# Kernel tuning notes

Measured on AMD Instinct MI355X. Metric: run time of the kernel, lower is better.

Reference implementation:

```python
import jax, jax.numpy as jnp
import numpy as np
import math

D_MODEL = 1024
N_HEAD = 16
D_K = D_MODEL // N_HEAD  # 64
SEQ = 1024
BATCH = 8


def setup_inputs() -> dict:
    k = jax.random.key(0)
    ks = jax.random.split(k, 11)
    f32 = jnp.float32
    scale = 1.0 / math.sqrt(D_MODEL)
    return {
        "query": jax.random.normal(ks[0], (BATCH, SEQ, D_MODEL), dtype=f32),
        "key": jax.random.normal(ks[1], (BATCH, SEQ, D_MODEL), dtype=f32),
        "value": jax.random.normal(ks[2], (BATCH, SEQ, D_MODEL), dtype=f32),
        # Shaw-style relative position table a[q_pos, k_pos, d_k]
        "rel": jax.random.normal(ks[3], (SEQ, SEQ, D_K), dtype=f32) * 0.02,
        "W_q": jax.random.normal(ks[4], (D_MODEL, D_MODEL), dtype=f32) * scale,
        "b_q": jnp.zeros((D_MODEL,), dtype=f32),
        "W_k": jax.random.normal(ks[5], (D_MODEL, D_MODEL), dtype=f32) * scale,
        "b_k": jnp.zeros((D_MODEL,), dtype=f32),
        "W_v": jax.random.normal(ks[6], (D_MODEL, D_MODEL), dtype=f32) * scale,
        "b_v": jnp.zeros((D_MODEL,), dtype=f32),
        # boolean mask: True = masked out (matches torch masked_fill semantics)
        "mask": jax.random.randint(ks[7], (BATCH, SEQ, SEQ), 0, 4) == 0,
    }


def reference(query, key, value, rel, W_q, b_q, W_k, b_k, W_v, b_v, mask):
    B, S, D = query.shape
    H, dk = N_HEAD, D // N_HEAD

    def proj(x, W, b):
        # [B,S,D] -> [B,H,S,dk]
        return (x @ W + b).reshape(B, S, H, dk).transpose(0, 2, 1, 3)

    Q = proj(query, W_q, b_q)
    K = proj(key, W_k, b_k)
    V = proj(value, W_v, b_v)

    # E_1 = Q K^T / sqrt(d_k): [B,H,Sq,Sk]
    scores = jnp.einsum("bhqd,bhkd->bhqk", Q, K) / math.sqrt(dk)
    # E_2 = Q x relative_position (per query position), added UNscaled as in source
    scores = scores + jnp.einsum("bhqd,qkd->bhqk", Q, rel)
    # masked_fill(mask, -1e8)
    scores = jnp.where(mask[:, None, :, :], jnp.float32(-1e8), scores)
    attn = jax.nn.softmax(scores, axis=-1)
    out = jnp.einsum("bhqk,bhkd->bhqd", attn, V)  # [B,H,S,dk]
    return out.transpose(0, 2, 1, 3).reshape(B, S, D)
```

## Files before the change

kernel.cpp:

```cpp
#include <hip/hip_runtime.h>

typedef _Float16 h8_t __attribute__((ext_vector_type(8)));
typedef _Float16 h4_t __attribute__((ext_vector_type(4)));
typedef float f4_t __attribute__((ext_vector_type(4)));

#define MFMA16(a, b, c) __builtin_amdgcn_mfma_f32_16x16x32_f16((a), (b), (c), 0, 0, 0)

__global__ void cvt4(const float* __restrict__ in, _Float16* __restrict__ out, int n4) {
    int i = blockIdx.x * 256 + threadIdx.x;
    if (i < n4) {
        f4_t v = *(const f4_t*)(in + (size_t)i * 4);
        h4_t h;
        for (int j = 0; j < 4; ++j) h[j] = (_Float16)v[j];
        *(h4_t*)(out + (size_t)i * 4) = h;
    }
}

__global__ void wtrans(const float* __restrict__ W, _Float16* __restrict__ Wt) {
    __shared__ float tile[32][33];
    int tid = threadIdx.x;
    int tx = tid & 31, ty = tid >> 5;
    int nb = blockIdx.x * 32, kb = blockIdx.y * 32;
    for (int p = 0; p < 4; ++p)
        tile[ty + p * 8][tx] = W[(size_t)(kb + ty + p * 8) * 1024 + nb + tx];
    __syncthreads();
    for (int p = 0; p < 4; ++p)
        Wt[(size_t)(nb + ty + p * 8) * 1024 + kb + tx] = (_Float16)tile[tx][ty + p * 8];
}

__global__ __launch_bounds__(256, 2) void proj_gemm(
    const _Float16* __restrict__ X, const _Float16* __restrict__ Wt,
    const float* __restrict__ bias, _Float16* __restrict__ Out,
    float scale, int vmode)
{
    __shared__ __align__(16) _Float16 Asm[128][40];
    __shared__ __align__(16) _Float16 Bsm[128][40];
    int tid = threadIdx.x;
    int wave = tid >> 6, lane = tid & 63;
    int l15 = lane & 15, quad = lane >> 4;
    int m0 = blockIdx.x * 128, n0 = blockIdx.y * 128;
    int wm = (wave >> 1) * 64, wn = (wave & 1) * 64;
    f4_t acc[4][4] = {};
    int srow = tid >> 1, skoff = (tid & 1) * 16;

    for (int kt = 0; kt < 1024; kt += 32) {
        h8_t a0 = *(const h8_t*)&X[(size_t)(m0 + srow) * 1024 + kt + skoff];
        h8_t a1 = *(const h8_t*)&X[(size_t)(m0 + srow) * 1024 + kt + skoff + 8];
        h8_t b0 = *(const h8_t*)&Wt[(size_t)(n0 + srow) * 1024 + kt + skoff];
        h8_t b1 = *(const h8_t*)&Wt[(size_t)(n0 + srow) * 1024 + kt + skoff + 8];
        *(h8_t*)&Asm[srow][skoff] = a0;
        *(h8_t*)&Asm[srow][skoff + 8] = a1;
        *(h8_t*)&Bsm[srow][skoff] = b0;
        *(h8_t*)&Bsm[srow][skoff + 8] = b1;
        __syncthreads();
        h8_t af[4], bf[4];
        for (int i = 0; i < 4; ++i) af[i] = *(const h8_t*)&Asm[wm + i * 16 + l15][quad * 8];
        for (int j = 0; j < 4; ++j) bf[j] = *(const h8_t*)&Bsm[wn + j * 16 + l15][quad * 8];
        for (int i = 0; i < 4; ++i)
            for (int j = 0; j < 4; ++j)
                acc[i][j] = MFMA16(af[i], bf[j], acc[i][j]);
        __syncthreads();
    }
    for (int j = 0; j < 4; ++j) {
        int n = n0 + wn + j * 16 + l15;
        float bv = bias[n];
        int h = n >> 6, d = n & 63;
        for (int i = 0; i < 4; ++i) {
            for (int r = 0; r < 4; ++r) {
                int m = m0 + wm + i * 16 + quad * 4 + r;
                int bb = m >> 10, ss = m & 1023;
                float v = (acc[i][j][r] + bv) * scale;
                size_t oidx = vmode ? (((size_t)(bb * 16 + h) * 64 + d) * 1024 + ss)
                                    : (((size_t)(bb * 16 + h) * 1024 + ss) * 64 + d);
                Out[oidx] = (_Float16)v;
            }
        }
    }
}

__device__ inline h8_t ld_rel(const _Float16* relh, const float* relf, size_t idx) {
    if (relh) return *(const h8_t*)(relh + idx);
    f4_t a = *(const f4_t*)(relf + idx);
    f4_t b = *(const f4_t*)(relf + idx + 4);
    h8_t h;
    for (int j = 0; j < 4; ++j) { h[j] = (_Float16)a[j]; h[4 + j] = (_Float16)b[j]; }
    return h;
}

__global__ __launch_bounds__(256, 2) void attn_kernel(
    const _Float16* __restrict__ Qh,
    const _Float16* __restrict__ Kh,
    const _Float16* __restrict__ Vt,
    const _Float16* __restrict__ relh,
    const float* __restrict__ relf,
    const int* __restrict__ mask,
    float* __restrict__ out)
{
    __shared__ __align__(16) _Float16 R_lds[16][17][36];
    __shared__ __align__(16) _Float16 P_lds[16][16][40];

    const int tid = threadIdx.x;
    const int wave = tid >> 6, lane = tid & 63;
    const int l15 = lane & 15, quad = lane >> 4;
    const int b = blockIdx.y;
    const int q0 = blockIdx.x * 16;

    h8_t bQ[4][2];
    h8_t bR[4][2];
    for (int gi = 0; gi < 4; ++gi) {
        int g = wave * 4 + gi;
        const _Float16* qp = Qh + ((size_t)(b * 16 + g) * 1024 + q0 + l15) * 64 + quad * 8;
        bQ[gi][0] = *(const h8_t*)qp;
        bQ[gi][1] = *(const h8_t*)(qp + 32);
    }
    for (int qi = 0; qi < 4; ++qi) {
        int q = q0 + wave * 4 + qi;
        const _Float16* qp = Qh + ((size_t)(b * 16 + l15) * 1024 + q) * 64 + quad * 8;
        bR[qi][0] = *(const h8_t*)qp;
        bR[qi][1] = *(const h8_t*)(qp + 32);
    }

    f4_t acc[4][4] = {};
    float mst[4], lst[4];
    for (int gi = 0; gi < 4; ++gi) { mst[gi] = -1e30f; lst[gi] = 0.0f; }

    for (int t0 = 0; t0 < 1024; t0 += 32) {
        for (int qi = 0; qi < 4; ++qi) {
            int q = q0 + wave * 4 + qi;
            for (int tm = 0; tm < 2; ++tm) {
                f4_t c = {0.f, 0.f, 0.f, 0.f};
                size_t ridx = ((size_t)q * 1024 + t0 + tm * 16 + l15) * 64 + quad * 8;
                c = MFMA16(ld_rel(relh, relf, ridx), bR[qi][0], c);
                c = MFMA16(ld_rel(relh, relf, ridx + 32), bR[qi][1], c);
                h4_t h;
                for (int r = 0; r < 4; ++r) h[r] = (_Float16)c[r];
                *(h4_t*)&R_lds[wave * 4 + qi][l15][tm * 16 + quad * 4] = h;
            }
        }
        __syncthreads();

        int4 mk0 = *(const int4*)&mask[((size_t)b * 1024 + q0 + l15) * 1024 + t0 + quad * 4];
        int4 mk1 = *(const int4*)&mask[((size_t)b * 1024 + q0 + l15) * 1024 + t0 + 16 + quad * 4];
        int mm[8] = {mk0.x, mk0.y, mk0.z, mk0.w, mk1.x, mk1.y, mk1.z, mk1.w};

        for (int gi = 0; gi < 4; ++gi) {
            int g = wave * 4 + gi;
            f4_t s[2];
            for (int tm = 0; tm < 2; ++tm) {
                h4_t rh = *(const h4_t*)&R_lds[l15][g][tm * 16 + quad * 4];
                f4_t c;
                for (int r = 0; r < 4; ++r) c[r] = (float)rh[r];
                const _Float16* kp =
                    Kh + ((size_t)(b * 16 + g) * 1024 + t0 + tm * 16 + l15) * 64 + quad * 8;
                c = MFMA16(*(const h8_t*)kp, bQ[gi][0], c);
                c = MFMA16(*(const h8_t*)(kp + 32), bQ[gi][1], c);
                s[tm] = c;
            }
            for (int tm = 0; tm < 2; ++tm)
                for (int r = 0; r < 4; ++r)
                    if (mm[tm * 4 + r]) s[tm][r] = -1e8f;

            float mx = s[0][0];
            for (int tm = 0; tm < 2; ++tm)
                for (int r = 0; r < 4; ++r) mx = fmaxf(mx, s[tm][r]);
            mx = fmaxf(mx, __shfl_xor(mx, 16));
            mx = fmaxf(mx, __shfl_xor(mx, 32));
            float mnew = fmaxf(mst[gi], mx);
            float alpha = __expf(mst[gi] - mnew);
            mst[gi] = mnew;
            float rs = 0.0f;
            for (int tm = 0; tm < 2; ++tm)
                for (int r = 0; r < 4; ++r) {
                    float p = __expf(s[tm][r] - mnew);
                    s[tm][r] = p;
                    rs += p;
                }
            rs += __shfl_xor(rs, 16);
            rs += __shfl_xor(rs, 32);
            lst[gi] = lst[gi] * alpha + rs;
            for (int dm = 0; dm < 4; ++dm) acc[gi][dm] *= alpha;
            for (int tm = 0; tm < 2; ++tm) {
                h4_t h;
                for (int r = 0; r < 4; ++r) h[r] = (_Float16)s[tm][r];
                *(h4_t*)&P_lds[g][l15][tm * 16 + quad * 4] = h;
            }
        }
        __syncthreads();

        for (int gi = 0; gi < 4; ++gi) {
            int g = wave * 4 + gi;
            h8_t bp = *(const h8_t*)&P_lds[g][l15][quad * 8];
            const _Float16* vp = Vt + (size_t)(b * 16 + g) * 64 * 1024 + t0 + quad * 8;
            for (int dm = 0; dm < 4; ++dm) {
                h8_t av = *(const h8_t*)(vp + (size_t)(dm * 16 + l15) * 1024);
                acc[gi][dm] = MFMA16(av, bp, acc[gi][dm]);
            }
        }
    }

    for (int gi = 0; gi < 4; ++gi) {
        int g = wave * 4 + gi;
        float linv = 1.0f / lst[gi];
        for (int dm = 0; dm < 4; ++dm) {
            f4_t v = acc[gi][dm] * linv;
            float* op = out + ((size_t)b * 1024 + q0 + l15) * 1024 + g * 64 + dm * 16 + quad * 4;
            *(f4_t*)op = v;
        }
    }
}

extern "C" void kernel_launch(void* const* d_in, const int* in_sizes, int n_in,
                              void* d_out, int out_size, void* d_ws, size_t ws_size,
                              hipStream_t stream) {
    const float* q    = (const float*)d_in[0];
    const float* k    = (const float*)d_in[1];
    const float* v    = (const float*)d_in[2];
    const float* rel  = (const float*)d_in[3];
    const float* Wq   = (const float*)d_in[4];
    const float* bq   = (const float*)d_in[5];
    const float* Wk   = (const float*)d_in[6];
    const float* bk   = (const float*)d_in[7];
    const float* Wv   = (const float*)d_in[8];
    const float* bv   = (const float*)d_in[9];
    const int*   mask = (const int*)d_in[10];
    float* out = (float*)d_out;

    const size_t NEL = 8ull * 1024 * 1024;
    const size_t WEL = 1024ull * 1024;
    const size_t RELE = 1024ull * 1024 * 64;

    char* w = (char*)d_ws;
    size_t off = 0;
    auto alloc = [&](size_t bytes) { char* p = w + off; off += bytes; return p; };
    _Float16* qx  = (_Float16*)alloc(NEL * 2);
    _Float16* kx  = (_Float16*)alloc(NEL * 2);
    _Float16* vx  = (_Float16*)alloc(NEL * 2);
    _Float16* Wqt = (_Float16*)alloc(WEL * 2);
    _Float16* Wkt = (_Float16*)alloc(WEL * 2);
    _Float16* Wvt = (_Float16*)alloc(WEL * 2);
    _Float16* Qh  = (_Float16*)alloc(NEL * 2);
    _Float16* Kh  = (_Float16*)alloc(NEL * 2);
    _Float16* Vth = (_Float16*)alloc(NEL * 2);
    _Float16* relh = nullptr;
    if (ws_size >= off + RELE * 2) relh = (_Float16*)alloc(RELE * 2);

    cvt4<<<(int)(NEL / 4 / 256), 256, 0, stream>>>(q, qx, (int)(NEL / 4));
    cvt4<<<(int)(NEL / 4 / 256), 256, 0, stream>>>(k, kx, (int)(NEL / 4));
    cvt4<<<(int)(NEL / 4 / 256), 256, 0, stream>>>(v, vx, (int)(NEL / 4));
    if (relh)
        cvt4<<<(int)(RELE / 4 / 256), 256, 0, stream>>>(rel, relh, (int)(RELE / 4));

    dim3 tg(32, 32);
    wtrans<<<tg, 256, 0, stream>>>(Wq, Wqt);
    wtrans<<<tg, 256, 0, stream>>>(Wk, Wkt);
    wtrans<<<tg, 256, 0, stream>>>(Wv, Wvt);

    dim3 pg(64, 8);
    proj_gemm<<<pg, 256, 0, stream>>>(qx, Wqt, bq, Qh, 1.0f, 0);
    proj_gemm<<<pg, 256, 0, stream>>>(kx, Wkt, bk, Kh, 0.125f, 0);
    proj_gemm<<<pg, 256, 0, stream>>>(vx, Wvt, bv, Vth, 1.0f, 1);

    dim3 ag(64, 8);
    attn_kernel<<<ag, 256, 0, stream>>>(Qh, Kh, Vth, relh, rel, mask, out);
}
```

Baseline: 1.067 ms.

## Prefetch attention operands, double-buffer R tile, use direct global-to-LDS loads in projection

In the attention kernel, the mask, relative-position, K and V tiles are now loaded into registers in batches ahead of the MFMAs that use them. The R scratch buffer is double-buffered, which lets the barrier before the P·V step go, since each wave only reads back its own P rows. This is meant to expose more memory-level parallelism and cut barrier stalls on a loop that is bound by loads. The projection GEMM switches to global_load_lds with an unpadded 32-wide LDS layout. That removes the register round trip but may add LDS bank conflicts on the fragment reads, and the extra prefetch registers raise register pressure.

```diff
diff --git a/kernel.cpp b/kernel.cpp
--- a/kernel.cpp
+++ b/kernel.cpp
@@ -5,6 +5,12 @@
 typedef float f4_t __attribute__((ext_vector_type(4)));
 
 #define MFMA16(a, b, c) __builtin_amdgcn_mfma_f32_16x16x32_f16((a), (b), (c), 0, 0, 0)
+
+__device__ inline void gl_lds16(const _Float16* g, _Float16* l) {
+    __builtin_amdgcn_global_load_lds(
+        (const __attribute__((address_space(1))) unsigned int*)g,
+        (__attribute__((address_space(3))) unsigned int*)l, 16, 0, 0);
+}
 
 __global__ void cvt4(const float* __restrict__ in, _Float16* __restrict__ out, int n4) {
     int i = blockIdx.x * 256 + threadIdx.x;
@@ -33,29 +39,27 @@
     const float* __restrict__ bias, _Float16* __restrict__ Out,
     float scale, int vmode)
 {
-    __shared__ __align__(16) _Float16 Asm[128][40];
-    __shared__ __align__(16) _Float16 Bsm[128][40];
+    __shared__ __align__(16) _Float16 Asm[128 * 32];
+    __shared__ __align__(16) _Float16 Bsm[128 * 32];
     int tid = threadIdx.x;
     int wave = tid >> 6, lane = tid & 63;
     int l15 = lane & 15, quad = lane >> 4;
     int m0 = blockIdx.x * 128, n0 = blockIdx.y * 128;
     int wm = (wave >> 1) * 64, wn = (wave & 1) * 64;
     f4_t acc[4][4] = {};
-    int srow = tid >> 1, skoff = (tid & 1) * 16;
+    int f0 = wave * 128 + lane;
 
     for (int kt = 0; kt < 1024; kt += 32) {
-        h8_t a0 = *(const h8_t*)&X[(size_t)(m0 + srow) * 1024 + kt + skoff];
-        h8_t a1 = *(const h8_t*)&X[(size_t)(m0 + srow) * 1024 + kt + skoff + 8];
-        h8_t b0 = *(const h8_t*)&Wt[(size_t)(n0 + srow) * 1024 + kt + skoff];
-        h8_t b1 = *(const h8_t*)&Wt[(size_t)(n0 + srow) * 1024 + kt + skoff + 8];
-        *(h8_t*)&Asm[srow][skoff] = a0;
-        *(h8_t*)&Asm[srow][skoff + 8] = a1;
-        *(h8_t*)&Bsm[srow][skoff] = b0;
-        *(h8_t*)&Bsm[srow][skoff + 8] = b1;
+        for (int j = 0; j < 2; ++j) {
+            int f = f0 + j * 64;
+            int r = f >> 2, c = (f & 3) * 8;
+            gl_lds16(&X[(size_t)(m0 + r) * 1024 + kt + c], &Asm[f * 8]);
+            gl_lds16(&Wt[(size_t)(n0 + r) * 1024 + kt + c], &Bsm[f * 8]);
+        }
         __syncthreads();
         h8_t af[4], bf[4];
-        for (int i = 0; i < 4; ++i) af[i] = *(const h8_t*)&Asm[wm + i * 16 + l15][quad * 8];
-        for (int j = 0; j < 4; ++j) bf[j] = *(const h8_t*)&Bsm[wn + j * 16 + l15][quad * 8];
+        for (int i = 0; i < 4; ++i) af[i] = *(const h8_t*)&Asm[(wm + i * 16 + l15) * 32 + quad * 8];
+        for (int j = 0; j < 4; ++j) bf[j] = *(const h8_t*)&Bsm[(wn + j * 16 + l15) * 32 + quad * 8];
         for (int i = 0; i < 4; ++i)
             for (int j = 0; j < 4; ++j)
                 acc[i][j] = MFMA16(af[i], bf[j], acc[i][j]);
@@ -96,7 +100,7 @@
     const int* __restrict__ mask,
     float* __restrict__ out)
 {
-    __shared__ __align__(16) _Float16 R_lds[16][17][36];
+    __shared__ __align__(16) _Float16 R_lds[2][16][17][36];
     __shared__ __align__(16) _Float16 P_lds[16][16][40];
 
     const int tid = threadIdx.x;
@@ -124,36 +128,53 @@
     float mst[4], lst[4];
     for (int gi = 0; gi < 4; ++gi) { mst[gi] = -1e30f; lst[gi] = 0.0f; }
 
-    for (int t0 = 0; t0 < 1024; t0 += 32) {
+    int buf = 0;
+    for (int t0 = 0; t0 < 1024; t0 += 32, buf ^= 1) {
+        const int* mrow = &mask[((size_t)b * 1024 + q0 + l15) * 1024 + t0];
+        int4 mk0 = *(const int4*)(mrow + quad * 4);
+        int4 mk1 = *(const int4*)(mrow + 16 + quad * 4);
+
+        h8_t relv[4][2][2];
         for (int qi = 0; qi < 4; ++qi) {
-            int q = q0 + wave * 4 + qi;
+            size_t rb = ((size_t)(q0 + wave * 4 + qi) * 1024 + t0 + l15) * 64 + quad * 8;
+            relv[qi][0][0] = ld_rel(relh, relf, rb);
+            relv[qi][0][1] = ld_rel(relh, relf, rb + 32);
+            relv[qi][1][0] = ld_rel(relh, relf, rb + 1024);
+            relv[qi][1][1] = ld_rel(relh, relf, rb + 1056);
+        }
+        for (int qi = 0; qi < 4; ++qi) {
             for (int tm = 0; tm < 2; ++tm) {
                 f4_t c = {0.f, 0.f, 0.f, 0.f};
-                size_t ridx = ((size_t)q * 1024 + t0 + tm * 16 + l15) * 64 + quad * 8;
-                c = MFMA16(ld_rel(relh, relf, ridx), bR[qi][0], c);
-                c = MFMA16(ld_rel(relh, relf, ridx + 32), bR[qi][1], c);
+                c = MFMA16(relv[qi][tm][0], bR[qi][0], c);
+                c = MFMA16(relv[qi][tm][1], bR[qi][1], c);
                 h4_t h;
                 for (int r = 0; r < 4; ++r) h[r] = (_Float16)c[r];
-                *(h4_t*)&R_lds[wave * 4 + qi][l15][tm * 16 + quad * 4] = h;
-            }
+                *(h4_t*)&R_lds[buf][wave * 4 + qi][l15][tm * 16 + quad * 4] = h;
+            }
+        }
+
+        h8_t kv[4][2][2];
+        for (int gi = 0; gi < 4; ++gi) {
+            const _Float16* kp =
+                Kh + ((size_t)(b * 16 + wave * 4 + gi) * 1024 + t0 + l15) * 64 + quad * 8;
+            kv[gi][0][0] = *(const h8_t*)kp;
+            kv[gi][0][1] = *(const h8_t*)(kp + 32);
+            kv[gi][1][0] = *(const h8_t*)(kp + 1024);
+            kv[gi][1][1] = *(const h8_t*)(kp + 1056);
         }
         __syncthreads();
 
-        int4 mk0 = *(const int4*)&mask[((size_t)b * 1024 + q0 + l15) * 1024 + t0 + quad * 4];
-        int4 mk1 = *(const int4*)&mask[((size_t)b * 1024 + q0 + l15) * 1024 + t0 + 16 + quad * 4];
         int mm[8] = {mk0.x, mk0.y, mk0.z, mk0.w, mk1.x, mk1.y, mk1.z, mk1.w};
 
         for (int gi = 0; gi < 4; ++gi) {
             int g = wave * 4 + gi;
             f4_t s[2];
             for (int tm = 0; tm < 2; ++tm) {
-                h4_t rh = *(const h4_t*)&R_lds[l15][g][tm * 16 + quad * 4];
+                h4_t rh = *(const h4_t*)&R_lds[buf][l15][g][tm * 16 + quad * 4];
                 f4_t c;
                 for (int r = 0; r < 4; ++r) c[r] = (float)rh[r];
-                const _Float16* kp =
-                    Kh + ((size_t)(b * 16 + g) * 1024 + t0 + tm * 16 + l15) * 64 + quad * 8;
-                c = MFMA16(*(const h8_t*)kp, bQ[gi][0], c);
-                c = MFMA16(*(const h8_t*)(kp + 32), bQ[gi][1], c);
+                c = MFMA16(kv[gi][tm][0], bQ[gi][0], c);
+                c = MFMA16(kv[gi][tm][1], bQ[gi][1], c);
                 s[tm] = c;
             }
             for (int tm = 0; tm < 2; ++tm)
@@ -185,16 +206,18 @@
                 *(h4_t*)&P_lds[g][l15][tm * 16 + quad * 4] = h;
             }
         }
-        __syncthreads();
-
-        for (int gi = 0; gi < 4; ++gi) {
-            int g = wave * 4 + gi;
-            h8_t bp = *(const h8_t*)&P_lds[g][l15][quad * 8];
-            const _Float16* vp = Vt + (size_t)(b * 16 + g) * 64 * 1024 + t0 + quad * 8;
-            for (int dm = 0; dm < 4; ++dm) {
-                h8_t av = *(const h8_t*)(vp + (size_t)(dm * 16 + l15) * 1024);
-                acc[gi][dm] = MFMA16(av, bp, acc[gi][dm]);
-            }
+
+        h8_t vv[4][4];
+        for (int gi = 0; gi < 4; ++gi) {
+            const _Float16* vp =
+                Vt + (size_t)(b * 16 + wave * 4 + gi) * 65536 + t0 + quad * 8;
+            for (int dm = 0; dm < 4; ++dm)
+                vv[gi][dm] = *(const h8_t*)(vp + (size_t)(dm * 16 + l15) * 1024);
+        }
+        for (int gi = 0; gi < 4; ++gi) {
+            h8_t bp = *(const h8_t*)&P_lds[wave * 4 + gi][l15][quad * 8];
+            for (int dm = 0; dm < 4; ++dm)
+                acc[gi][dm] = MFMA16(vv[gi][dm], bp, acc[gi][dm]);
         }
     }
 
```

After: 943.2 us. -11.6%, faster.
